# Optimization experiments

Measured on AMD Instinct MI355X. Metric: run time of the kernel, lower is better.

## Reference

```python
import jax, jax.numpy as jnp
import numpy as np

B, V, NB, NJ, NEXTRA = 512, 6890, 10, 24, 9
PARENTS = np.array([-1,0,0,0,1,2,3,4,5,6,7,8,9,9,9,12,13,14,16,17,18,19,20,21], dtype=np.int32)


def setup_inputs() -> dict:
    key = jax.random.key(0)
    ks = jax.random.split(key, 11)
    betas = jax.random.normal(ks[0], (B, NB + 1), jnp.float32) * 0.1
    betas = betas.at[:, 0].set(1.0)  # col 0 is a global scale in this SMPL variant
    body_pose = jax.random.normal(ks[1], (B, 3 * (NJ - 1)), jnp.float32) * 0.2
    global_orient = jax.random.normal(ks[2], (B, 3), jnp.float32) * 0.2
    transl = jax.random.normal(ks[3], (B, 3), jnp.float32) * 0.1
    model_scale_opt = jnp.ones((1,), jnp.float32)
    smpl_v_template = jax.random.normal(ks[4], (V, 3), jnp.float32)
    smil_v_template = jax.random.normal(ks[5], (V, 3), jnp.float32)
    shapedirs = jax.random.normal(ks[6], (V, 3, NB), jnp.float32) * 0.01
    J_regressor = jax.nn.softmax(jax.random.normal(ks[7], (NJ, V), jnp.float32), axis=1)
    lbs_weights = jax.nn.softmax(jax.random.normal(ks[8], (V, NJ), jnp.float32) * 4.0, axis=1)
    J_regressor_extra = jax.nn.softmax(jax.random.normal(ks[9], (NEXTRA, V), jnp.float32), axis=1)
    parents = jnp.asarray(PARENTS)
    return dict(betas=betas, body_pose=body_pose, global_orient=global_orient,
                transl=transl, model_scale_opt=model_scale_opt,
                smpl_v_template=smpl_v_template, smil_v_template=smil_v_template,
                shapedirs=shapedirs, J_regressor=J_regressor, lbs_weights=lbs_weights,
                J_regressor_extra=J_regressor_extra, parents=parents)


def batch_rodrigues(rvecs):
    # rvecs: [N,3] axis-angle -> [N,3,3] rotation matrices
    angle = jnp.linalg.norm(rvecs + 1e-8, axis=1, keepdims=True)  # [N,1]
    axis = rvecs / angle
    c = jnp.cos(angle)[..., None]  # [N,1,1]
    s = jnp.sin(angle)[..., None]
    rx, ry, rz = axis[:, 0], axis[:, 1], axis[:, 2]
    z = jnp.zeros_like(rx)
    K = jnp.stack([z, -rz, ry, rz, z, -rx, -ry, rx, z], axis=1).reshape(-1, 3, 3)
    I = jnp.eye(3, dtype=rvecs.dtype)
    return I + s * K + (1.0 - c) * jnp.matmul(K, K)


def _smpl_forward(betas, body_pose, global_orient, transl, model_scale_opt,
                  smpl_v_template, smil_v_template, shapedirs,
                  J_regressor, lbs_weights, J_regressor_extra):
    dtype = betas.dtype
    # ---- updateShape ----
    s = model_scale_opt[0]
    v_template = smpl_v_template * s + (1.0 - s) * smil_v_template  # [V,3]
    blend_shape = jnp.einsum('bl,mkl->bmk', betas[:, 1:], shapedirs)  # [B,V,3]
    v_shaped = (v_template[None] + blend_shape) * betas[:, :1, None]  # scale col
    J_shaped = jnp.einsum('bik,ji->bjk', v_shaped, J_regressor)  # [B,NJ,3]

    # ---- updatePose ----
    full_pose = jnp.concatenate([global_orient, body_pose], axis=1)  # [B,NJ*3]
    rot_mats = batch_rodrigues(full_pose.reshape(-1, 3)).reshape(B, NJ, 3, 3)

    # relative joint locations w.r.t. parents
    rel_joints = J_shaped.at[:, 1:].add(-J_shaped[:, PARENTS[1:]])
    top = jnp.concatenate([rot_mats, rel_joints[..., None]], axis=-1)  # [B,NJ,3,4]
    bottom = jnp.broadcast_to(
        jnp.array([0.0, 0.0, 0.0, 1.0], dtype=dtype), (B, NJ, 1, 4))
    mats = jnp.concatenate([top, bottom], axis=2)  # [B,NJ,4,4]

    # sequential kinematic-chain composition over the 24-joint tree
    chain = [mats[:, 0]]
    for i in range(1, NJ):
        chain.append(jnp.matmul(chain[PARENTS[i]], mats[:, i]))
    chain = jnp.stack(chain, axis=1)  # [B,NJ,4,4]
    posed_joints = chain[:, :, :3, 3]  # [B,NJ,3]

    # relative transforms: subtract rotated rest joints
    corr = jnp.einsum('bjmn,bjn->bjm', chain[:, :, :3, :3], J_shaped)
    A = chain.at[:, :, :3, 3].add(-corr)  # [B,NJ,4,4]

    # linear blend skinning
    T = jnp.einsum('vj,bjmn->bvmn', lbs_weights, A)  # [B,V,4,4]
    verts = jnp.einsum('bvmn,bvn->bvm', T[:, :, :3, :3], v_shaped) + T[:, :, :3, 3]

    extra_joints = jnp.einsum('bik,ji->bjk', verts, J_regressor_extra)  # [B,9,3]
    joints = jnp.concatenate([posed_joints, extra_joints], axis=1)  # [B,33,3]

    t = transl[:, None, :]
    # concat verts and joints along point dim for a single output array
    return jnp.concatenate([verts + t, joints + t], axis=1)  # [B, V+33, 3]


def reference(betas, body_pose, global_orient, transl, model_scale_opt,
              smpl_v_template, smil_v_template, shapedirs,
              J_regressor, lbs_weights, J_regressor_extra, parents):
    return _smpl_forward(betas, body_pose, global_orient, transl, model_scale_opt,
                         smpl_v_template, smil_v_template, shapedirs,
                         J_regressor, lbs_weights, J_regressor_extra)
```

## Files before the change

### kernel.cpp

```cpp
#include <hip/hip_runtime.h>


#define BATCH 512
#define NV 6890
#define NBD 10
#define NJ 24
#define NEXTRA 9
#define NOUT (NV + NJ + NEXTRA)
#define VBLK ((NV + 255) / 256)
#define BPB 4

__constant__ int c_par[NJ] = {-1,0,0,0,1,2,3,4,5,6,7,8,9,9,9,12,13,14,16,17,18,19,20,21};

__global__ __launch_bounds__(256) void precompute_kernel(
    const float* __restrict__ jreg,
    const float* __restrict__ smpl_t,
    const float* __restrict__ smil_t,
    const float* __restrict__ sdirs,
    const float* __restrict__ msc,
    float* __restrict__ jtjs)
{
    const int j = blockIdx.y;
    const int v = blockIdx.x * 256 + threadIdx.x;
    const float s = msc[0];

    float acc[33];
#pragma unroll
    for (int i = 0; i < 33; ++i) acc[i] = 0.f;

    if (v < NV) {
        const float w = jreg[j * NV + v];
#pragma unroll
        for (int k = 0; k < 3; ++k) {
            float vt = s * smpl_t[v * 3 + k] + (1.f - s) * smil_t[v * 3 + k];
            acc[k] = w * vt;
        }
        const float2* sd2 = (const float2*)(sdirs + (size_t)v * 30);
#pragma unroll
        for (int i = 0; i < 15; ++i) {
            float2 x = sd2[i];
            acc[3 + 2 * i]     = w * x.x;
            acc[3 + 2 * i + 1] = w * x.y;
        }
    }

#pragma unroll
    for (int i = 0; i < 33; ++i) {
        float x = acc[i];
        for (int off = 32; off; off >>= 1) x += __shfl_xor(x, off, 64);
        acc[i] = x;
    }

    __shared__ float red[4][33];
    const int lane = threadIdx.x & 63, wv = threadIdx.x >> 6;
    if (lane == 0) {
#pragma unroll
        for (int i = 0; i < 33; ++i) red[wv][i] = acc[i];
    }
    __syncthreads();
    if (threadIdx.x < 33) {
        float sum = red[0][threadIdx.x] + red[1][threadIdx.x]
                  + red[2][threadIdx.x] + red[3][threadIdx.x];
        atomicAdd(&jtjs[j * 33 + threadIdx.x], sum);
    }
}

__global__ __launch_bounds__(64) void joints_kernel(
    const float* __restrict__ betas,
    const float* __restrict__ body_pose,
    const float* __restrict__ glob_or,
    const float* __restrict__ transl,
    const float* __restrict__ jtjs,
    float* __restrict__ wsA,
    float* __restrict__ out)
{
    const int b = blockIdx.x;
    const int j = threadIdx.x;

    __shared__ float sJ[NJ][3];
    __shared__ float mats[NJ][12];
    __shared__ float chain[NJ][12];
    __shared__ float sbeta[NBD + 1];

    if (threadIdx.x < NBD + 1) sbeta[threadIdx.x] = betas[b * (NBD + 1) + threadIdx.x];
    __syncthreads();

    if (j < NJ) {
        const float beta0 = sbeta[0];
#pragma unroll
        for (int k = 0; k < 3; ++k) {
            float a = jtjs[j * 33 + k];
#pragma unroll
            for (int l = 0; l < NBD; ++l) a = fmaf(sbeta[1 + l], jtjs[j * 33 + 3 + k * 10 + l], a);
            sJ[j][k] = a * beta0;
        }
        float rx, ry, rz;
        if (j == 0) {
            rx = glob_or[b * 3 + 0]; ry = glob_or[b * 3 + 1]; rz = glob_or[b * 3 + 2];
        } else {
            rx = body_pose[b * 69 + (j - 1) * 3 + 0];
            ry = body_pose[b * 69 + (j - 1) * 3 + 1];
            rz = body_pose[b * 69 + (j - 1) * 3 + 2];
        }
        float ex = rx + 1e-8f, ey = ry + 1e-8f, ez = rz + 1e-8f;
        float ang = sqrtf(ex * ex + ey * ey + ez * ez);
        float inv = 1.f / ang;
        float ax = rx * inv, ay = ry * inv, az = rz * inv;
        float c = cosf(ang), s = sinf(ang), t = 1.f - c;
        mats[j][0]  = 1.f + t * (-(ay * ay + az * az));
        mats[j][1]  = -s * az + t * (ax * ay);
        mats[j][2]  =  s * ay + t * (ax * az);
        mats[j][4]  =  s * az + t * (ax * ay);
        mats[j][5]  = 1.f + t * (-(ax * ax + az * az));
        mats[j][6]  = -s * ax + t * (ay * az);
        mats[j][8]  = -s * ay + t * (ax * az);
        mats[j][9]  =  s * ax + t * (ay * az);
        mats[j][10] = 1.f + t * (-(ax * ax + ay * ay));
    }
    __syncthreads();
    if (j < NJ) {
        const int p = c_par[j];
        float t0 = sJ[j][0], t1 = sJ[j][1], t2 = sJ[j][2];
        if (p >= 0) { t0 -= sJ[p][0]; t1 -= sJ[p][1]; t2 -= sJ[p][2]; }
        mats[j][3] = t0; mats[j][7] = t1; mats[j][11] = t2;
    }
    __syncthreads();
    if (threadIdx.x == 0) {
#pragma unroll
        for (int k = 0; k < 12; ++k) chain[0][k] = mats[0][k];
        for (int i = 1; i < NJ; ++i) {
            const int p = c_par[i];
#pragma unroll
            for (int r = 0; r < 3; ++r) {
#pragma unroll
                for (int col = 0; col < 4; ++col) {
                    float acc = (col == 3) ? chain[p][r * 4 + 3] : 0.f;
#pragma unroll
                    for (int q = 0; q < 3; ++q) acc = fmaf(chain[p][r * 4 + q], mats[i][q * 4 + col], acc);
                    chain[i][r * 4 + col] = acc;
                }
            }
        }
    }
    __syncthreads();
    if (j < NJ) {
        float A[12];
#pragma unroll
        for (int k = 0; k < 12; ++k) A[k] = chain[j][k];
        const float c0 = A[3], c1 = A[7], c2 = A[11];
        const float j0 = sJ[j][0], j1 = sJ[j][1], j2 = sJ[j][2];
        A[3]  = c0 - (A[0] * j0 + A[1] * j1 + A[2]  * j2);
        A[7]  = c1 - (A[4] * j0 + A[5] * j1 + A[6]  * j2);
        A[11] = c2 - (A[8] * j0 + A[9] * j1 + A[10] * j2);
#pragma unroll
        for (int k = 0; k < 12; ++k) wsA[((size_t)b * NJ + j) * 12 + k] = A[k];
        const float tx = transl[b * 3 + 0], ty = transl[b * 3 + 1], tz = transl[b * 3 + 2];
        const size_t o = ((size_t)b * NOUT + NV + j) * 3;
        out[o + 0] = c0 + tx; out[o + 1] = c1 + ty; out[o + 2] = c2 + tz;
    }
}

__global__ __launch_bounds__(256) void lbs_kernel(
    const float* __restrict__ betas,
    const float* __restrict__ transl,
    const float* __restrict__ msc,
    const float* __restrict__ smpl_t,
    const float* __restrict__ smil_t,
    const float* __restrict__ sdirs,
    const float* __restrict__ lbsw,
    const float* __restrict__ wsA,
    float* __restrict__ out)
{
    const int v = blockIdx.x * 256 + threadIdx.x;
    const bool valid = v < NV;
    const int vc = valid ? v : NV - 1;
    const int b0 = blockIdx.y * BPB;
    const float s = msc[0];

    float vt[3];
#pragma unroll
    for (int k = 0; k < 3; ++k)
        vt[k] = s * smpl_t[vc * 3 + k] + (1.f - s) * smil_t[vc * 3 + k];

    float sd[30];
    {
        const float2* sd2 = (const float2*)(sdirs + (size_t)vc * 30);
#pragma unroll
        for (int i = 0; i < 15; ++i) { float2 x = sd2[i]; sd[2 * i] = x.x; sd[2 * i + 1] = x.y; }
    }
    float w[NJ];
    {
        const float4* w4 = (const float4*)(lbsw + (size_t)vc * NJ);
#pragma unroll
        for (int i = 0; i < 6; ++i) {
            float4 x = w4[i];
            w[4 * i] = x.x; w[4 * i + 1] = x.y; w[4 * i + 2] = x.z; w[4 * i + 3] = x.w;
        }
    }

#pragma unroll
    for (int bb = 0; bb < BPB; ++bb) {
        const int b = b0 + bb;
        const float* __restrict__ Bb = betas + b * (NBD + 1);
        const float* __restrict__ Ab = wsA + (size_t)b * NJ * 12;

        float vs[3];
#pragma unroll
        for (int k = 0; k < 3; ++k) {
            float a = vt[k];
#pragma unroll
            for (int l = 0; l < NBD; ++l) a = fmaf(Bb[1 + l], sd[k * 10 + l], a);
            vs[k] = a * Bb[0];
        }

        float T[12];
#pragma unroll
        for (int k = 0; k < 12; ++k) T[k] = 0.f;
#pragma unroll 4
        for (int jj = 0; jj < NJ; ++jj) {
            const float ww = w[jj];
#pragma unroll
            for (int k = 0; k < 12; ++k) T[k] = fmaf(ww, Ab[jj * 12 + k], T[k]);
        }

        if (valid) {
            const float tx = transl[b * 3 + 0], ty = transl[b * 3 + 1], tz = transl[b * 3 + 2];
            const size_t o = ((size_t)b * NOUT + v) * 3;
            out[o + 0] = fmaf(T[0], vs[0], fmaf(T[1], vs[1], fmaf(T[2],  vs[2], T[3])))  + tx;
            out[o + 1] = fmaf(T[4], vs[0], fmaf(T[5], vs[1], fmaf(T[6],  vs[2], T[7])))  + ty;
            out[o + 2] = fmaf(T[8], vs[0], fmaf(T[9], vs[1], fmaf(T[10], vs[2], T[11]))) + tz;
        }
    }
}

__global__ __launch_bounds__(256) void extra_kernel(
    const float* __restrict__ jre,
    float* out)
{
    const int b = blockIdx.x;
    const float* vb = out + (size_t)b * NOUT * 3;

    float acc[27];
#pragma unroll
    for (int i = 0; i < 27; ++i) acc[i] = 0.f;

    for (int v = threadIdx.x; v < NV; v += 256) {
        const float x = vb[v * 3 + 0], y = vb[v * 3 + 1], z = vb[v * 3 + 2];
#pragma unroll
        for (int e = 0; e < NEXTRA; ++e) {
            const float we = jre[e * NV + v];
            acc[e * 3 + 0] = fmaf(we, x, acc[e * 3 + 0]);
            acc[e * 3 + 1] = fmaf(we, y, acc[e * 3 + 1]);
            acc[e * 3 + 2] = fmaf(we, z, acc[e * 3 + 2]);
        }
    }

#pragma unroll
    for (int i = 0; i < 27; ++i) {
        float x = acc[i];
        for (int off = 32; off; off >>= 1) x += __shfl_xor(x, off, 64);
        acc[i] = x;
    }
    __shared__ float red[4][27];
    const int lane = threadIdx.x & 63, wv = threadIdx.x >> 6;
    if (lane == 0) {
#pragma unroll
        for (int i = 0; i < 27; ++i) red[wv][i] = acc[i];
    }
    __syncthreads();
    if (threadIdx.x < 27) {
        const float sum = red[0][threadIdx.x] + red[1][threadIdx.x]
                        + red[2][threadIdx.x] + red[3][threadIdx.x];
        out[((size_t)b * NOUT + NV + NJ) * 3 + threadIdx.x] = sum;
    }
}

extern "C" void kernel_launch(void* const* d_in, const int* in_sizes, int n_in,
                              void* d_out, int out_size, void* d_ws, size_t ws_size,
                              hipStream_t stream) {
    const float* betas     = (const float*)d_in[0];
    const float* body_pose = (const float*)d_in[1];
    const float* glob_or   = (const float*)d_in[2];
    const float* transl    = (const float*)d_in[3];
    const float* msc       = (const float*)d_in[4];
    const float* smpl_t    = (const float*)d_in[5];
    const float* smil_t    = (const float*)d_in[6];
    const float* sdirs     = (const float*)d_in[7];
    const float* jreg      = (const float*)d_in[8];
    const float* lbsw      = (const float*)d_in[9];
    const float* jre       = (const float*)d_in[10];

    float* out  = (float*)d_out;
    float* ws   = (float*)d_ws;
    float* jtjs = ws;
    float* wsA  = ws + 792;

    hipMemsetAsync(jtjs, 0, NJ * 33 * sizeof(float), stream);

    dim3 gA(VBLK, NJ);
    precompute_kernel<<<gA, 256, 0, stream>>>(jreg, smpl_t, smil_t, sdirs, msc, jtjs);

    joints_kernel<<<BATCH, 64, 0, stream>>>(betas, body_pose, glob_or, transl, jtjs, wsA, out);

    dim3 gC(VBLK, BATCH / BPB);
    lbs_kernel<<<gC, 256, 0, stream>>>(betas, transl, msc, smpl_t, smil_t, sdirs, lbsw, wsA, out);

    extra_kernel<<<BATCH, 256, 0, stream>>>(jre, out);
}
```

Measured before the change: 187.6 us.

## Process two vertices per thread in LBS and split extra-joint reduction across blocks

The LBS kernel now handles two vertices per thread, so each loaded joint transform element is reused for two vertices, and it fully unrolls the joint loop under a launch-bounds occupancy hint. The extra-joint regression kernel is split into four vertex chunks per batch item whose partial sums are combined with atomicAdd. The joints kernel zero-initialises the extra-joint output slots to support this. The changes raise parallelism and reuse but increase register pressure and make the summation order nondeterministic.

```diff
diff --git a/kernel.cpp b/kernel.cpp
--- a/kernel.cpp
+++ b/kernel.cpp
@@ -9,6 +9,10 @@
 #define NOUT (NV + NJ + NEXTRA)
 #define VBLK ((NV + 255) / 256)
 #define BPB 4
+#define VPT 2
+#define VSPAN (256 * VPT)
+#define NXB ((NV + VSPAN - 1) / VSPAN)
+#define ECHUNK ((NV + 3) / 4)
 
 __constant__ int c_par[NJ] = {-1,0,0,0,1,2,3,4,5,6,7,8,9,9,9,12,13,14,16,17,18,19,20,21};
 
@@ -83,6 +87,10 @@
     __shared__ float sbeta[NBD + 1];
 
     if (threadIdx.x < NBD + 1) sbeta[threadIdx.x] = betas[b * (NBD + 1) + threadIdx.x];
+
+    if (threadIdx.x >= NJ && threadIdx.x < NJ + 3 * NEXTRA)
+        out[((size_t)b * NOUT + NV + NJ) * 3 + (threadIdx.x - NJ)] = 0.f;
+
     __syncthreads();
 
     if (j < NJ) {
@@ -160,7 +168,7 @@
     }
 }
 
-__global__ __launch_bounds__(256) void lbs_kernel(
+__global__ __launch_bounds__(256, 3) void lbs_kernel(
     const float* __restrict__ betas,
     const float* __restrict__ transl,
     const float* __restrict__ msc,
@@ -171,64 +179,90 @@
     const float* __restrict__ wsA,
     float* __restrict__ out)
 {
-    const int v = blockIdx.x * 256 + threadIdx.x;
-    const bool valid = v < NV;
-    const int vc = valid ? v : NV - 1;
+    const int tid = threadIdx.x;
     const int b0 = blockIdx.y * BPB;
     const float s = msc[0];
 
-    float vt[3];
-#pragma unroll
-    for (int k = 0; k < 3; ++k)
-        vt[k] = s * smpl_t[vc * 3 + k] + (1.f - s) * smil_t[vc * 3 + k];
-
-    float sd[30];
-    {
-        const float2* sd2 = (const float2*)(sdirs + (size_t)vc * 30);
-#pragma unroll
-        for (int i = 0; i < 15; ++i) { float2 x = sd2[i]; sd[2 * i] = x.x; sd[2 * i + 1] = x.y; }
-    }
-    float w[NJ];
-    {
-        const float4* w4 = (const float4*)(lbsw + (size_t)vc * NJ);
+    int  vv[VPT];
+    bool val[VPT];
+    int  vc[VPT];
+#pragma unroll
+    for (int p = 0; p < VPT; ++p) {
+        vv[p]  = blockIdx.x * VSPAN + p * 256 + tid;
+        val[p] = vv[p] < NV;
+        vc[p]  = val[p] ? vv[p] : NV - 1;
+    }
+
+    float vt[VPT][3], w[VPT][NJ], sd[VPT][30];
+#pragma unroll
+    for (int p = 0; p < VPT; ++p) {
+#pragma unroll
+        for (int k = 0; k < 3; ++k)
+            vt[p][k] = s * smpl_t[vc[p] * 3 + k] + (1.f - s) * smil_t[vc[p] * 3 + k];
+        const float4* w4 = (const float4*)(lbsw + (size_t)vc[p] * NJ);
 #pragma unroll
         for (int i = 0; i < 6; ++i) {
             float4 x = w4[i];
-            w[4 * i] = x.x; w[4 * i + 1] = x.y; w[4 * i + 2] = x.z; w[4 * i + 3] = x.w;
-        }
-    }
-
-#pragma unroll
+            w[p][4 * i]     = x.x; w[p][4 * i + 1] = x.y;
+            w[p][4 * i + 2] = x.z; w[p][4 * i + 3] = x.w;
+        }
+        const float2* sd2 = (const float2*)(sdirs + (size_t)vc[p] * 30);
+#pragma unroll
+        for (int i = 0; i < 15; ++i) { float2 x = sd2[i]; sd[p][2 * i] = x.x; sd[p][2 * i + 1] = x.y; }
+    }
+#pragma unroll
+    for (int p = 0; p < VPT; ++p)
+#pragma unroll
+        for (int i = 0; i < NJ; ++i) asm("" : "+v"(w[p][i]));
+
     for (int bb = 0; bb < BPB; ++bb) {
         const int b = b0 + bb;
         const float* __restrict__ Bb = betas + b * (NBD + 1);
         const float* __restrict__ Ab = wsA + (size_t)b * NJ * 12;
 
-        float vs[3];
-#pragma unroll
-        for (int k = 0; k < 3; ++k) {
-            float a = vt[k];
-#pragma unroll
-            for (int l = 0; l < NBD; ++l) a = fmaf(Bb[1 + l], sd[k * 10 + l], a);
-            vs[k] = a * Bb[0];
-        }
-
-        float T[12];
-#pragma unroll
-        for (int k = 0; k < 12; ++k) T[k] = 0.f;
-#pragma unroll 4
+        const float beta0 = Bb[0];
+        float bet[NBD];
+#pragma unroll
+        for (int l = 0; l < NBD; ++l) bet[l] = Bb[1 + l];
+
+        float vs[VPT][3];
+#pragma unroll
+        for (int p = 0; p < VPT; ++p) {
+#pragma unroll
+            for (int k = 0; k < 3; ++k) {
+                float a = vt[p][k];
+#pragma unroll
+                for (int l = 0; l < NBD; ++l) a = fmaf(bet[l], sd[p][k * 10 + l], a);
+                vs[p][k] = a * beta0;
+            }
+        }
+
+        float T[VPT][12];
+#pragma unroll
+        for (int p = 0; p < VPT; ++p)
+#pragma unroll
+            for (int k = 0; k < 12; ++k) T[p][k] = 0.f;
+
+#pragma unroll
         for (int jj = 0; jj < NJ; ++jj) {
-            const float ww = w[jj];
-#pragma unroll
-            for (int k = 0; k < 12; ++k) T[k] = fmaf(ww, Ab[jj * 12 + k], T[k]);
-        }
-
-        if (valid) {
-            const float tx = transl[b * 3 + 0], ty = transl[b * 3 + 1], tz = transl[b * 3 + 2];
-            const size_t o = ((size_t)b * NOUT + v) * 3;
-            out[o + 0] = fmaf(T[0], vs[0], fmaf(T[1], vs[1], fmaf(T[2],  vs[2], T[3])))  + tx;
-            out[o + 1] = fmaf(T[4], vs[0], fmaf(T[5], vs[1], fmaf(T[6],  vs[2], T[7])))  + ty;
-            out[o + 2] = fmaf(T[8], vs[0], fmaf(T[9], vs[1], fmaf(T[10], vs[2], T[11]))) + tz;
+#pragma unroll
+            for (int k = 0; k < 12; ++k) {
+                const float a = Ab[jj * 12 + k];
+#pragma unroll
+                for (int p = 0; p < VPT; ++p)
+                    T[p][k] = fmaf(w[p][jj], a, T[p][k]);
+            }
+        }
+
+        const float tx = transl[b * 3 + 0], ty = transl[b * 3 + 1], tz = transl[b * 3 + 2];
+#pragma unroll
+        for (int p = 0; p < VPT; ++p) {
+            if (val[p]) {
+                const size_t o = ((size_t)b * NOUT + vv[p]) * 3;
+                out[o + 0] = fmaf(T[p][0], vs[p][0], fmaf(T[p][1], vs[p][1], fmaf(T[p][2],  vs[p][2],  T[p][3])))  + tx;
+                out[o + 1] = fmaf(T[p][4], vs[p][0], fmaf(T[p][5], vs[p][1], fmaf(T[p][6],  vs[p][2],  T[p][7])))  + ty;
+                out[o + 2] = fmaf(T[p][8], vs[p][0], fmaf(T[p][9], vs[p][1], fmaf(T[p][10], vs[p][2],  T[p][11]))) + tz;
+            }
         }
     }
 }
@@ -237,14 +271,16 @@
     const float* __restrict__ jre,
     float* out)
 {
-    const int b = blockIdx.x;
+    const int b = blockIdx.y;
+    const int v0 = blockIdx.x * ECHUNK;
+    int vend = v0 + ECHUNK; if (vend > NV) vend = NV;
     const float* vb = out + (size_t)b * NOUT * 3;
 
     float acc[27];
 #pragma unroll
     for (int i = 0; i < 27; ++i) acc[i] = 0.f;
 
-    for (int v = threadIdx.x; v < NV; v += 256) {
+    for (int v = v0 + threadIdx.x; v < vend; v += 256) {
         const float x = vb[v * 3 + 0], y = vb[v * 3 + 1], z = vb[v * 3 + 2];
 #pragma unroll
         for (int e = 0; e < NEXTRA; ++e) {
@@ -271,7 +307,7 @@
     if (threadIdx.x < 27) {
         const float sum = red[0][threadIdx.x] + red[1][threadIdx.x]
                         + red[2][threadIdx.x] + red[3][threadIdx.x];
-        out[((size_t)b * NOUT + NV + NJ) * 3 + threadIdx.x] = sum;
+        atomicAdd(&out[((size_t)b * NOUT + NV + NJ) * 3 + threadIdx.x], sum);
     }
 }
 
@@ -302,8 +338,9 @@
 
     joints_kernel<<<BATCH, 64, 0, stream>>>(betas, body_pose, glob_or, transl, jtjs, wsA, out);
 
-    dim3 gC(VBLK, BATCH / BPB);
+    dim3 gC(NXB, BATCH / BPB);
     lbs_kernel<<<gC, 256, 0, stream>>>(betas, transl, msc, smpl_t, smil_t, sdirs, lbsw, wsA, out);
 
-    extra_kernel<<<BATCH, 256, 0, stream>>>(jre, out);
-}
+    dim3 gE(4, BATCH);
+    extra_kernel<<<gE, 256, 0, stream>>>(jre, out);
+}
```

Measured after the change: 307.1 us. 63.7% more time.
